# Performance work log

Measured on AMD Instinct MI355X. Metric: run time of the kernel, lower is better.

Reference implementation:

```python
import jax, jax.numpy as jnp
import numpy as np

K = 8
DIM = 64
NUM_BLOCKS = 12
BN_EPS = 1e-5
LRELU_SLOPE = 0.01  # torch nn.LeakyReLU default negative_slope


def knn_indices(xyz, k):
    # xyz: [b, 3, n] -> idx [b, n, k] of k nearest neighbors (self included)
    x = jnp.transpose(xyz, (0, 2, 1))  # [b, n, 3]
    sq = jnp.sum(x * x, axis=-1)  # [b, n]
    d2 = sq[:, :, None] - 2.0 * jnp.einsum('bnd,bmd->bnm', x, x) + sq[:, None, :]
    _, idx = jax.lax.top_k(-d2, k)  # k smallest distances
    return idx


def group_point(points, idx):
    # points [b, d, n], idx [b, n, k] -> grouped [b, d, k, n]
    g = jax.vmap(lambda p, i: p[:, i])(points, idx)  # [b, d, n, k]
    return jnp.transpose(g, (0, 1, 3, 2))


def setup_inputs() -> dict:
    key = jax.random.key(0)
    ks = jax.random.split(key, 6)
    b, n = 8, 4096
    xyz = jax.random.normal(ks[0], (b, 3, n), dtype=jnp.float32)
    points = jax.random.normal(ks[1], (b, DIM, n), dtype=jnp.float32)
    # per-block params (note: the module's second Conv2d per block is never used
    # in forward — layers[4*idx+2] is applied to both center and grouped points)
    conv_w = jax.random.normal(ks[2], (NUM_BLOCKS, DIM, DIM), dtype=jnp.float32) * (1.0 / np.sqrt(DIM))
    conv_b = jax.random.normal(ks[3], (NUM_BLOCKS, DIM), dtype=jnp.float32) * 0.01
    bn_gamma = 1.0 + 0.1 * jax.random.normal(ks[4], (NUM_BLOCKS, DIM), dtype=jnp.float32)
    bn_beta = 0.1 * jax.random.normal(ks[5], (NUM_BLOCKS, DIM), dtype=jnp.float32)
    return {"xyz": xyz, "points": points, "conv_w": conv_w, "conv_b": conv_b,
            "bn_gamma": bn_gamma, "bn_beta": bn_beta}


def reference(xyz, points, conv_w, conv_b, bn_gamma, bn_beta):
    idx = knn_indices(xyz, K)  # fixed graph, computed once in block 0

    def block(p, params):
        w, b, g, be = params  # [DIM,DIM], [DIM], [DIM], [DIM]
        shortcut = p
        # BatchNorm1d (training-mode batch stats over batch & point dims)
        mean = jnp.mean(p, axis=(0, 2), keepdims=True)
        var = jnp.var(p, axis=(0, 2), keepdims=True)
        h = (p - mean) * jax.lax.rsqrt(var + BN_EPS) * g[None, :, None] + be[None, :, None]
        # LeakyReLU
        h = jnp.where(h >= 0, h, LRELU_SLOPE * h)
        # gather neighbor features: [b, d, k, n]
        grouped = group_point(h, idx)
        # shared 1x1 conv on center and grouped points
        center = jnp.einsum('od,bdn->bon', w, h) + b[None, :, None]            # [b,d,n]
        gconv = jnp.einsum('od,bdkn->bokn', w, grouped) + b[None, :, None, None]  # [b,d,k,n]
        # mean over concat([center[:, :, None], gconv], axis=2) == (center + sum_k gconv) / (k+1)
        new_p = (center + jnp.sum(gconv, axis=2)) / (K + 1) + shortcut
        return new_p, None

    out, _ = jax.lax.scan(block, points, (conv_w, conv_b, bn_gamma, bn_beta))
    return out
```

## Files before the change

kernel.cpp:

```cpp
#include <hip/hip_runtime.h>
#include <hip/hip_bf16.h>

#define NB     8
#define NPTS   4096
#define DIMC   64
#define KNN_K  8
#define NBLK   12
#define NREP   8

typedef __attribute__((ext_vector_type(8))) short short8;
typedef __attribute__((ext_vector_type(4))) float f32x4;

__device__ __forceinline__ void bsplit(float v, unsigned short& h, unsigned short& l) {
    unsigned b = __float_as_uint(v);
    h = (unsigned short)(b >> 16);
    float hf = __uint_as_float(b & 0xFFFF0000u);
    float lf = v - hf;
    l = (unsigned short)(__float_as_uint(lf) >> 16);
}

__global__ __launch_bounds__(256) void prep_kernel(
        const float* __restrict__ xyz, float4* __restrict__ pts4g,
        float* __restrict__ stats) {
#pragma clang fp contract(off)
    int g = blockIdx.x * 256 + threadIdx.x;
    if (g < 13 * NREP * 128) stats[g] = 0.0f;
    int b = g >> 12, j = g & 4095;
    const float* xb = xyz + (size_t)b * 3 * NPTS;
    float x = xb[j];
    float y = xb[NPTS + j];
    float z = xb[2 * NPTS + j];
    float sq = (x * x + y * y) + z * z;
    pts4g[g] = make_float4(x, y, z, sq);
}

__global__ __launch_bounds__(256) void cast_kernel(
        const float* __restrict__ pts,
        float* __restrict__ P0, float* __restrict__ stats0) {
    __shared__ __align__(16) float tr[64 * 65];
    __shared__ float slotA[4 * 64], slotB[4 * 64];
    int wg = blockIdx.x;
    int b = wg & 7;
    int n0 = (wg >> 3) << 6;
    int rep = (wg >> 3) & (NREP - 1);
    int tid = threadIdx.x;
    int lane6 = tid & 63;
    int grp = tid >> 6;

    #pragma unroll
    for (int k = 0; k < 16; ++k) {
        int d = grp + (k << 2);
        float v = pts[(((size_t)((b << 6) + d)) << 12) + n0 + lane6];
        tr[d * 65 + lane6] = v;
    }
    __syncthreads();
    int c = lane6;
    float s = 0.0f, s2 = 0.0f;
    #pragma unroll
    for (int k = 0; k < 16; ++k) {
        int p = grp + (k << 2);
        float v = tr[c * 65 + p];
        P0[((size_t)((b << 12) + n0 + p)) * 64 + c] = v;
        s += v; s2 += v * v;
    }
    slotA[grp * 64 + c] = s;
    slotB[grp * 64 + c] = s2;
    __syncthreads();
    if (tid < 64) {
        float t = slotA[tid] + slotA[64 + tid] + slotA[128 + tid] + slotA[192 + tid];
        atomicAdd(&stats0[rep * 128 + tid], t);
    } else if (tid < 128) {
        int cc = tid - 64;
        float t = slotB[cc] + slotB[64 + cc] + slotB[128 + cc] + slotB[192 + cc];
        atomicAdd(&stats0[rep * 128 + 64 + cc], t);
    }
}

#define INS(KEY) do { \
    double key = (KEY); \
    double n0 = fmin(k0, key); \
    double n1 = fmin(k1, fmax(k0, key)); \
    double n2 = fmin(k2, fmax(k1, key)); \
    double n3 = fmin(k3, fmax(k2, key)); \
    double n4 = fmin(k4, fmax(k3, key)); \
    double n5 = fmin(k5, fmax(k4, key)); \
    double n6 = fmin(k6, fmax(k5, key)); \
    double n7 = fmin(k7, fmax(k6, key)); \
    k0 = n0; k1 = n1; k2 = n2; k3 = n3; \
    k4 = n4; k5 = n5; k6 = n6; k7 = n7; } while (0)

__global__ __launch_bounds__(512) void knn_kernel(
        const float4* __restrict__ pts4g, int* __restrict__ idx) {
#pragma clang fp contract(off)
    __shared__ double stash[4 * 9 * 128];
    int wg = blockIdx.x;
    int b = wg >> 5;
    int q0 = (wg & 31) << 7;
    int tid = threadIdx.x;

    int lane  = tid & 63;
    int wave  = tid >> 6;
    int chunk = wave & 3;
    int qgrp  = wave >> 2;
    int q_l   = (qgrp << 6) | lane;

    const float4* cb = pts4g + ((size_t)b << 12);
    float4 qp = cb[q0 + q_l];

    double k0, k1, k2, k3, k4, k5, k6, k7;
    k0 = k1 = k2 = k3 = k4 = k5 = k6 = k7 = __builtin_inf();
    float bd7f = 3.4e38f;

    int chu = __builtin_amdgcn_readfirstlane(chunk);
    const float4* cc = cb + ((size_t)chu << 10);
    int jg0 = chu << 10;

    for (int jo = 0; jo < 128; jo += 8) {
        float d2v[8];
        #pragma unroll
        for (int u = 0; u < 8; ++u) {
            float4 p = cc[jo + u];
            float dot = (qp.x * p.x + qp.y * p.y) + qp.z * p.z;
            d2v[u] = (qp.w - 2.0f * dot) + p.w;
        }
        #pragma unroll
        for (int u = 0; u < 8; ++u) {
            unsigned long long kb =
                __double_as_longlong((double)d2v[u]) |
                (unsigned long long)(jg0 + jo + u);
            INS(__longlong_as_double(kb));
        }
    }
    bd7f = (float)k7;

    for (int jo = 128; jo < 1024; jo += 8) {
        float d2v[8];
        unsigned hm = 0u;
        #pragma unroll
        for (int u = 0; u < 8; ++u) {
            float4 p = cc[jo + u];
            float dot = (qp.x * p.x + qp.y * p.y) + qp.z * p.z;
            float d2 = (qp.w - 2.0f * dot) + p.w;
            d2v[u] = d2;
            hm |= (d2 < bd7f) ? (1u << u) : 0u;
        }
        while (__any(hm != 0u)) {
            if (hm) {
                int u = __builtin_ctz(hm);
                hm &= hm - 1u;
                float t0 = (u & 1) ? d2v[1] : d2v[0];
                float t1 = (u & 1) ? d2v[3] : d2v[2];
                float t2 = (u & 1) ? d2v[5] : d2v[4];
                float t3 = (u & 1) ? d2v[7] : d2v[6];
                float s0 = (u & 2) ? t1 : t0;
                float s1 = (u & 2) ? t3 : t2;
                float d2 = (u & 4) ? s1 : s0;
                unsigned long long kb =
                    __double_as_longlong((double)d2) |
                    (unsigned long long)(jg0 + jo + u);
                INS(__longlong_as_double(kb));
            }
        }
        bd7f = (float)k7;
    }

    {
        double* S = &stash[(chunk * 9) * 128 + q_l];
        S[0 * 128] = k0; S[1 * 128] = k1; S[2 * 128] = k2; S[3 * 128] = k3;
        S[4 * 128] = k4; S[5 * 128] = k5; S[6 * 128] = k6; S[7 * 128] = k7;
        S[8 * 128] = __builtin_inf();
    }
    __syncthreads();

    if (tid < 128) {
        int h0 = 0, h1 = 0, h2 = 0, h3 = 0;
        int* op = idx + ((size_t)(b * NPTS + q0 + tid)) * 8;
        #pragma unroll
        for (int t = 0; t < 8; ++t) {
            double b0 = stash[(0 * 9 + h0) * 128 + tid];
            double b1 = stash[(1 * 9 + h1) * 128 + tid];
            double b2 = stash[(2 * 9 + h2) * 128 + tid];
            double b3 = stash[(3 * 9 + h3) * 128 + tid];
            double best = b0; int bc = 0;
            if (b1 < best) { best = b1; bc = 1; }
            if (b2 < best) { best = b2; bc = 2; }
            if (b3 < best) { best = b3; bc = 3; }
            h0 += (bc == 0); h1 += (bc == 1);
            h2 += (bc == 2); h3 += (bc == 3);
            op[t] = (int)(__double_as_longlong(best) & 0xFFFULL);
        }
    }
}

#define AH_OFF 0
#define AL_OFF (64 * 72)
#define WH_OFF (2 * 64 * 72)
#define WL_OFF (3 * 64 * 72)

__global__ __launch_bounds__(256) void block_kernel(
        const float* __restrict__ Pin, float* __restrict__ Pout,
        const float* __restrict__ statsIn, float* __restrict__ statsOut,
        const float* __restrict__ Wp, const float* __restrict__ Bp,
        const float* __restrict__ Gp, const float* __restrict__ Betap,
        const int* __restrict__ gidx, float* __restrict__ dout, int last) {
    __shared__ __align__(16) unsigned short planes[4 * 64 * 72];
    __shared__ __align__(16) float selft[64 * 64];
    __shared__ __align__(16) int   idxl[64 * 8];
    __shared__ __align__(16) float scale_l[64], shift_l[64], bias_l[64];
    __shared__ float slot[4 * 128];

    int wg = blockIdx.x;
    int b = wg & 7;
    int n0 = (wg >> 3) << 6;
    int rep = (wg >> 3) & (NREP - 1);
    int tid = threadIdx.x;

    const float* Pb = Pin + (((size_t)b) << 18);

    if (tid < 128) {
        ((int4*)idxl)[tid] = ((const int4*)(gidx + ((size_t)(b * NPTS + n0)) * 8))[tid];
    }
    #pragma unroll
    for (int k = 0; k < 4; ++k) {
        int lin = tid + (k << 8);
        ((float4*)selft)[lin] = ((const float4*)&Pb[(size_t)n0 << 6])[lin];
    }
    #pragma unroll
    for (int k = 0; k < 4; ++k) {
        int lin = tid + (k << 8);
        float4 wv = ((const float4*)Wp)[lin];
        int o = lin >> 4, d4 = (lin & 15) << 2;
        unsigned short hx, hy, hz, hw, lx, ly, lz, lw;
        bsplit(wv.x, hx, lx); bsplit(wv.y, hy, ly);
        bsplit(wv.z, hz, lz); bsplit(wv.w, hw, lw);
        *(ushort4*)&planes[WH_OFF + o * 72 + d4] = make_ushort4(hx, hy, hz, hw);
        *(ushort4*)&planes[WL_OFF + o * 72 + d4] = make_ushort4(lx, ly, lz, lw);
    }
    if (tid < 64) {
        int c = tid;
        float sum = 0.0f, sumsq = 0.0f;
        #pragma unroll
        for (int r = 0; r < NREP; ++r) {
            sum   += statsIn[r * 128 + c];
            sumsq += statsIn[r * 128 + 64 + c];
        }
        float mean = sum * (1.0f / 32768.0f);
        float var  = sumsq * (1.0f / 32768.0f) - mean * mean;
        float rs   = 1.0f / sqrtf(var + 1e-5f);
        float sc   = Gp[c] * rs;
        scale_l[c] = sc;
        shift_l[c] = Betap[c] - mean * sc;
        bias_l[c]  = Bp[c];
    }
    __syncthreads();

    {
        int cq = tid & 15;
        int pg = tid >> 4;
        int c4 = cq << 2;
        float4 sc4 = *(const float4*)&scale_l[c4];
        float4 sh4 = *(const float4*)&shift_l[c4];
        #pragma unroll
        for (int i = 0; i < 4; ++i) {
            int pt = (pg << 2) + i;
            int4 ja = *(const int4*)&idxl[pt * 8];
            int4 jb = *(const int4*)&idxl[pt * 8 + 4];
            float4 v[9];
            v[0] = *(const float4*)&selft[(pt << 6) + c4];
            v[1] = *(const float4*)&Pb[(((size_t)ja.x) << 6) + c4];
            v[2] = *(const float4*)&Pb[(((size_t)ja.y) << 6) + c4];
            v[3] = *(const float4*)&Pb[(((size_t)ja.z) << 6) + c4];
            v[4] = *(const float4*)&Pb[(((size_t)ja.w) << 6) + c4];
            v[5] = *(const float4*)&Pb[(((size_t)jb.x) << 6) + c4];
            v[6] = *(const float4*)&Pb[(((size_t)jb.y) << 6) + c4];
            v[7] = *(const float4*)&Pb[(((size_t)jb.z) << 6) + c4];
            v[8] = *(const float4*)&Pb[(((size_t)jb.w) << 6) + c4];
            float4 a = make_float4(0.f, 0.f, 0.f, 0.f);
            #pragma unroll
            for (int k = 0; k < 9; ++k) {
                float hx = v[k].x * sc4.x + sh4.x;
                float hy = v[k].y * sc4.y + sh4.y;
                float hz = v[k].z * sc4.z + sh4.z;
                float hw = v[k].w * sc4.w + sh4.w;
                a.x += fmaxf(hx, 0.01f * hx);
                a.y += fmaxf(hy, 0.01f * hy);
                a.z += fmaxf(hz, 0.01f * hz);
                a.w += fmaxf(hw, 0.01f * hw);
            }
            float mx = a.x * (1.0f / 9.0f), my = a.y * (1.0f / 9.0f);
            float mz = a.z * (1.0f / 9.0f), mw = a.w * (1.0f / 9.0f);
            unsigned short hx2, hy2, hz2, hw2, lx2, ly2, lz2, lw2;
            bsplit(mx, hx2, lx2); bsplit(my, hy2, ly2);
            bsplit(mz, hz2, lz2); bsplit(mw, hw2, lw2);
            *(ushort4*)&planes[AH_OFF + pt * 72 + c4] = make_ushort4(hx2, hy2, hz2, hw2);
            *(ushort4*)&planes[AL_OFF + pt * 72 + c4] = make_ushort4(lx2, ly2, lz2, lw2);
        }
    }
    __syncthreads();

    int lane = tid & 63;
    int w    = tid >> 6;
    int g    = lane >> 4;
    int c    = lane & 15;
    int ptb  = w << 4;

    short8 a_h[2], a_l[2];
    #pragma unroll
    for (int s = 0; s < 2; ++s) {
        int off = (ptb + c) * 72 + (s << 5) + (g << 3);
        a_h[s] = *(const short8*)&planes[AH_OFF + off];
        a_l[s] = *(const short8*)&planes[AL_OFF + off];
    }

    f32x4 out[4];
    #pragma unroll
    for (int ot = 0; ot < 4; ++ot) {
        int co = (ot << 4) + c;
        short8 b_h[2], b_l[2];
        #pragma unroll
        for (int s = 0; s < 2; ++s) {
            int off = co * 72 + (s << 5) + (g << 3);
            b_h[s] = *(const short8*)&planes[WH_OFF + off];
            b_l[s] = *(const short8*)&planes[WL_OFF + off];
        }
        f32x4 acc = {0.f, 0.f, 0.f, 0.f};
        acc = __builtin_amdgcn_mfma_f32_16x16x32_bf16(a_h[0], b_h[0], acc, 0, 0, 0);
        acc = __builtin_amdgcn_mfma_f32_16x16x32_bf16(a_h[1], b_h[1], acc, 0, 0, 0);
        acc = __builtin_amdgcn_mfma_f32_16x16x32_bf16(a_h[0], b_l[0], acc, 0, 0, 0);
        acc = __builtin_amdgcn_mfma_f32_16x16x32_bf16(a_h[1], b_l[1], acc, 0, 0, 0);
        acc = __builtin_amdgcn_mfma_f32_16x16x32_bf16(a_l[0], b_h[0], acc, 0, 0, 0);
        acc = __builtin_amdgcn_mfma_f32_16x16x32_bf16(a_l[1], b_h[1], acc, 0, 0, 0);
        out[ot] = acc;
    }

    #pragma unroll
    for (int ot = 0; ot < 4; ++ot) {
        int co = (ot << 4) + c;
        float bv = bias_l[co];
        #pragma unroll
        for (int j = 0; j < 4; ++j) {
            int pt = ptb + (g << 2) + j;
            out[ot][j] += bv + selft[(pt << 6) + co];
        }
    }

    if (!last) {
        float* PbOut = Pout + ((((size_t)b) << 12) + n0) * 64;
        #pragma unroll
        for (int j = 0; j < 4; ++j) {
            int pt = ptb + (g << 2) + j;
            #pragma unroll
            for (int ot = 0; ot < 4; ++ot)
                PbOut[(size_t)pt * 64 + (ot << 4) + c] = out[ot][j];
        }

        float sv[4], qv[4];
        #pragma unroll
        for (int ot = 0; ot < 4; ++ot) {
            float s = 0.f, q = 0.f;
            #pragma unroll
            for (int j = 0; j < 4; ++j) {
                float v = out[ot][j];
                s += v; q += v * v;
            }
            sv[ot] = s; qv[ot] = q;
        }
        #pragma unroll
        for (int m = 16; m <= 32; m <<= 1) {
            #pragma unroll
            for (int ot = 0; ot < 4; ++ot) {
                sv[ot] += __shfl_xor(sv[ot], m, 64);
                qv[ot] += __shfl_xor(qv[ot], m, 64);
            }
        }
        if (lane < 16) {
            #pragma unroll
            for (int ot = 0; ot < 4; ++ot) {
                slot[w * 128 + (ot << 4) + lane]      = sv[ot];
                slot[w * 128 + 64 + (ot << 4) + lane] = qv[ot];
            }
        }
        __syncthreads();
        if (tid < 128) {
            float t = slot[tid] + slot[128 + tid] + slot[256 + tid] + slot[384 + tid];
            atomicAdd(&statsOut[rep * 128 + tid], t);
        }
    } else {
        __syncthreads();
        float* stage = (float*)planes;
        #pragma unroll
        for (int ot = 0; ot < 4; ++ot) {
            int co = (ot << 4) + c;
            #pragma unroll
            for (int j = 0; j < 4; ++j)
                stage[co * 65 + ptb + (g << 2) + j] = out[ot][j];
        }
        __syncthreads();
        #pragma unroll
        for (int k = 0; k < 16; ++k) {
            int lin = tid + (k << 8);
            int o = lin >> 6, pt = lin & 63;
            dout[(((size_t)((b << 6) + o)) << 12) + n0 + pt] = stage[o * 65 + pt];
        }
    }
}

extern "C" void kernel_launch(void* const* d_in, const int* in_sizes, int n_in,
                              void* d_out, int out_size, void* d_ws, size_t ws_size,
                              hipStream_t stream) {
    const float* xyz    = (const float*)d_in[0];
    const float* pts    = (const float*)d_in[1];
    const float* conv_w = (const float*)d_in[2];
    const float* conv_b = (const float*)d_in[3];
    const float* gamma  = (const float*)d_in[4];
    const float* beta   = (const float*)d_in[5];
    float* out = (float*)d_out;

    char* ws = (char*)d_ws;
    float*  P0    = (float*)(ws);
    float*  P1    = (float*)(ws + (size_t)8 * 1024 * 1024);
    int*    idx   = (int*)  (ws + (size_t)16 * 1024 * 1024);
    float*  stats = (float*)(ws + (size_t)17 * 1024 * 1024);
    float4* pts4g = (float4*)(ws + (size_t)18 * 1024 * 1024);

    prep_kernel<<<128, 256, 0, stream>>>(xyz, pts4g, stats);
    cast_kernel<<<512, 256, 0, stream>>>(pts, P0, stats);
    knn_kernel<<<256, 512, 0, stream>>>(pts4g, idx);

    float* Pbuf[2] = {P0, P1};
    for (int t = 0; t < NBLK; ++t) {
        block_kernel<<<512, 256, 0, stream>>>(
            Pbuf[t & 1], Pbuf[(t + 1) & 1],
            stats + (size_t)t * NREP * 128, stats + (size_t)(t + 1) * NREP * 128,
            conv_w + (size_t)t * 4096, conv_b + (size_t)t * 64,
            gamma + (size_t)t * 64, beta + (size_t)t * 64,
            idx, out, (t == NBLK - 1) ? 1 : 0);
    }
}
```

Measured before the change: 284.9 us.

## Precompute activated bf16 split features and run conv per neighbor before summing

Adds a separate h_kernel that applies BatchNorm and LeakyReLU once per point and writes the bf16 hi/lo planes to global memory. The block kernel then gathers those planes per neighbor and accumulates nine MFMA GEMMs, with the weights pre-split and pre-scaled by 1/9 in prep_kernel. Previously each point's 8 neighbors were normalized and activated redundantly before a single GEMM on the aggregated features. The trade is nine times the MFMA work, 12 extra kernel launches, and an extra global write and read of the h planes per block.

```diff
diff --git a/kernel.cpp b/kernel.cpp
--- a/kernel.cpp
+++ b/kernel.cpp
@@ -21,17 +21,28 @@
 
 __global__ __launch_bounds__(256) void prep_kernel(
         const float* __restrict__ xyz, float4* __restrict__ pts4g,
-        float* __restrict__ stats) {
+        float* __restrict__ stats, const float* __restrict__ conv_w,
+        unsigned short* __restrict__ wq) {
 #pragma clang fp contract(off)
     int g = blockIdx.x * 256 + threadIdx.x;
     if (g < 13 * NREP * 128) stats[g] = 0.0f;
-    int b = g >> 12, j = g & 4095;
-    const float* xb = xyz + (size_t)b * 3 * NPTS;
-    float x = xb[j];
-    float y = xb[NPTS + j];
-    float z = xb[2 * NPTS + j];
-    float sq = (x * x + y * y) + z * z;
-    pts4g[g] = make_float4(x, y, z, sq);
+    {
+        int t = g >> 12, rem = g & 4095;
+        float wv = conv_w[g] * (1.0f / 9.0f);
+        unsigned short h, l;
+        bsplit(wv, h, l);
+        wq[(t << 13) + rem]        = h;
+        wq[(t << 13) + 4096 + rem] = l;
+    }
+    if (g < 32768) {
+        int b = g >> 12, j = g & 4095;
+        const float* xb = xyz + (size_t)b * 3 * NPTS;
+        float x = xb[j];
+        float y = xb[NPTS + j];
+        float z = xb[2 * NPTS + j];
+        float sq = (x * x + y * y) + z * z;
+        pts4g[g] = make_float4(x, y, z, sq);
+    }
 }
 
 __global__ __launch_bounds__(256) void cast_kernel(
@@ -192,50 +203,16 @@
     }
 }
 
-#define AH_OFF 0
-#define AL_OFF (64 * 72)
-#define WH_OFF (2 * 64 * 72)
-#define WL_OFF (3 * 64 * 72)
-
-__global__ __launch_bounds__(256) void block_kernel(
-        const float* __restrict__ Pin, float* __restrict__ Pout,
-        const float* __restrict__ statsIn, float* __restrict__ statsOut,
-        const float* __restrict__ Wp, const float* __restrict__ Bp,
+__global__ __launch_bounds__(256) void h_kernel(
+        const float* __restrict__ P, const float* __restrict__ statsIn,
         const float* __restrict__ Gp, const float* __restrict__ Betap,
-        const int* __restrict__ gidx, float* __restrict__ dout, int last) {
-    __shared__ __align__(16) unsigned short planes[4 * 64 * 72];
-    __shared__ __align__(16) float selft[64 * 64];
-    __shared__ __align__(16) int   idxl[64 * 8];
-    __shared__ __align__(16) float scale_l[64], shift_l[64], bias_l[64];
-    __shared__ float slot[4 * 128];
-
+        unsigned short* __restrict__ hH, unsigned short* __restrict__ hL) {
+    __shared__ float scale_l[64], shift_l[64];
     int wg = blockIdx.x;
     int b = wg & 7;
     int n0 = (wg >> 3) << 6;
-    int rep = (wg >> 3) & (NREP - 1);
     int tid = threadIdx.x;
 
-    const float* Pb = Pin + (((size_t)b) << 18);
-
-    if (tid < 128) {
-        ((int4*)idxl)[tid] = ((const int4*)(gidx + ((size_t)(b * NPTS + n0)) * 8))[tid];
-    }
-    #pragma unroll
-    for (int k = 0; k < 4; ++k) {
-        int lin = tid + (k << 8);
-        ((float4*)selft)[lin] = ((const float4*)&Pb[(size_t)n0 << 6])[lin];
-    }
-    #pragma unroll
-    for (int k = 0; k < 4; ++k) {
-        int lin = tid + (k << 8);
-        float4 wv = ((const float4*)Wp)[lin];
-        int o = lin >> 4, d4 = (lin & 15) << 2;
-        unsigned short hx, hy, hz, hw, lx, ly, lz, lw;
-        bsplit(wv.x, hx, lx); bsplit(wv.y, hy, ly);
-        bsplit(wv.z, hz, lz); bsplit(wv.w, hw, lw);
-        *(ushort4*)&planes[WH_OFF + o * 72 + d4] = make_ushort4(hx, hy, hz, hw);
-        *(ushort4*)&planes[WL_OFF + o * 72 + d4] = make_ushort4(lx, ly, lz, lw);
-    }
     if (tid < 64) {
         int c = tid;
         float sum = 0.0f, sumsq = 0.0f;
@@ -250,51 +227,50 @@
         float sc   = Gp[c] * rs;
         scale_l[c] = sc;
         shift_l[c] = Betap[c] - mean * sc;
-        bias_l[c]  = Bp[c];
     }
     __syncthreads();
 
-    {
-        int cq = tid & 15;
-        int pg = tid >> 4;
-        int c4 = cq << 2;
-        float4 sc4 = *(const float4*)&scale_l[c4];
-        float4 sh4 = *(const float4*)&shift_l[c4];
-        #pragma unroll
-        for (int i = 0; i < 4; ++i) {
-            int pt = (pg << 2) + i;
-            int4 ja = *(const int4*)&idxl[pt * 8];
-            int4 jb = *(const int4*)&idxl[pt * 8 + 4];
-            float4 v[9];
-            v[0] = *(const float4*)&selft[(pt << 6) + c4];
-            v[1] = *(const float4*)&Pb[(((size_t)ja.x) << 6) + c4];
-            v[2] = *(const float4*)&Pb[(((size_t)ja.y) << 6) + c4];
-            v[3] = *(const float4*)&Pb[(((size_t)ja.z) << 6) + c4];
-            v[4] = *(const float4*)&Pb[(((size_t)ja.w) << 6) + c4];
-            v[5] = *(const float4*)&Pb[(((size_t)jb.x) << 6) + c4];
-            v[6] = *(const float4*)&Pb[(((size_t)jb.y) << 6) + c4];
-            v[7] = *(const float4*)&Pb[(((size_t)jb.z) << 6) + c4];
-            v[8] = *(const float4*)&Pb[(((size_t)jb.w) << 6) + c4];
-            float4 a = make_float4(0.f, 0.f, 0.f, 0.f);
-            #pragma unroll
-            for (int k = 0; k < 9; ++k) {
-                float hx = v[k].x * sc4.x + sh4.x;
-                float hy = v[k].y * sc4.y + sh4.y;
-                float hz = v[k].z * sc4.z + sh4.z;
-                float hw = v[k].w * sc4.w + sh4.w;
-                a.x += fmaxf(hx, 0.01f * hx);
-                a.y += fmaxf(hy, 0.01f * hy);
-                a.z += fmaxf(hz, 0.01f * hz);
-                a.w += fmaxf(hw, 0.01f * hw);
-            }
-            float mx = a.x * (1.0f / 9.0f), my = a.y * (1.0f / 9.0f);
-            float mz = a.z * (1.0f / 9.0f), mw = a.w * (1.0f / 9.0f);
-            unsigned short hx2, hy2, hz2, hw2, lx2, ly2, lz2, lw2;
-            bsplit(mx, hx2, lx2); bsplit(my, hy2, ly2);
-            bsplit(mz, hz2, lz2); bsplit(mw, hw2, lw2);
-            *(ushort4*)&planes[AH_OFF + pt * 72 + c4] = make_ushort4(hx2, hy2, hz2, hw2);
-            *(ushort4*)&planes[AL_OFF + pt * 72 + c4] = make_ushort4(lx2, ly2, lz2, lw2);
-        }
+    const float4* P4 = (const float4*)(P + (((size_t)(b << 12) + n0) << 6));
+    ushort4* h4 = (ushort4*)(hH + (((size_t)(b << 12) + n0) << 6));
+    ushort4* l4 = (ushort4*)(hL + (((size_t)(b << 12) + n0) << 6));
+    #pragma unroll
+    for (int k = 0; k < 4; ++k) {
+        int lin = tid + (k << 8);
+        int c4 = (lin & 15) << 2;
+        float4 v = P4[lin];
+        float hx = v.x * scale_l[c4 + 0] + shift_l[c4 + 0];
+        float hy = v.y * scale_l[c4 + 1] + shift_l[c4 + 1];
+        float hz = v.z * scale_l[c4 + 2] + shift_l[c4 + 2];
+        float hw = v.w * scale_l[c4 + 3] + shift_l[c4 + 3];
+        hx = fmaxf(hx, 0.01f * hx); hy = fmaxf(hy, 0.01f * hy);
+        hz = fmaxf(hz, 0.01f * hz); hw = fmaxf(hw, 0.01f * hw);
+        unsigned short ax, ay, az, aw, bx, by, bz, bw;
+        bsplit(hx, ax, bx); bsplit(hy, ay, by);
+        bsplit(hz, az, bz); bsplit(hw, aw, bw);
+        h4[lin] = make_ushort4(ax, ay, az, aw);
+        l4[lin] = make_ushort4(bx, by, bz, bw);
+    }
+}
+
+__global__ __launch_bounds__(256) void block_kernel(
+        const float* __restrict__ Pin, float* __restrict__ Pout,
+        float* __restrict__ statsOut,
+        const unsigned short* __restrict__ whl, const float* __restrict__ Bp,
+        const int* __restrict__ gidx,
+        const unsigned short* __restrict__ hH, const unsigned short* __restrict__ hL,
+        float* __restrict__ dout, int last) {
+    __shared__ __align__(16) int   idxl[64 * 8];
+    __shared__ float slot[4 * 128];
+    __shared__ __align__(16) float stage[64 * 65];
+
+    int wg = blockIdx.x;
+    int b = wg & 7;
+    int n0 = (wg >> 3) << 6;
+    int rep = (wg >> 3) & (NREP - 1);
+    int tid = threadIdx.x;
+
+    if (tid < 128) {
+        ((int4*)idxl)[tid] = ((const int4*)(gidx + ((size_t)(b * NPTS + n0)) * 8))[tid];
     }
     __syncthreads();
 
@@ -302,56 +278,67 @@
     int w    = tid >> 6;
     int g    = lane >> 4;
     int c    = lane & 15;
-    int ptb  = w << 4;
-
-    short8 a_h[2], a_l[2];
-    #pragma unroll
-    for (int s = 0; s < 2; ++s) {
-        int off = (ptb + c) * 72 + (s << 5) + (g << 3);
-        a_h[s] = *(const short8*)&planes[AH_OFF + off];
-        a_l[s] = *(const short8*)&planes[AL_OFF + off];
-    }
-
-    f32x4 out[4];
+    int ptl  = (w << 4) + c;
+
+    int r[9];
+    r[0] = n0 + ptl;
+    #pragma unroll
+    for (int j = 1; j < 9; ++j) r[j] = idxl[ptl * 8 + (j - 1)];
+
+    const unsigned short* hHb = hH + ((size_t)(b << 12) << 6);
+    const unsigned short* hLb = hL + ((size_t)(b << 12) << 6);
+    const unsigned short* whi = whl;
+    const unsigned short* wlo = whl + 4096;
+
+    short8 bh[4][2], bl[4][2];
     #pragma unroll
     for (int ot = 0; ot < 4; ++ot) {
         int co = (ot << 4) + c;
-        short8 b_h[2], b_l[2];
-        #pragma unroll
-        for (int s = 0; s < 2; ++s) {
-            int off = co * 72 + (s << 5) + (g << 3);
-            b_h[s] = *(const short8*)&planes[WH_OFF + off];
-            b_l[s] = *(const short8*)&planes[WL_OFF + off];
-        }
-        f32x4 acc = {0.f, 0.f, 0.f, 0.f};
-        acc = __builtin_amdgcn_mfma_f32_16x16x32_bf16(a_h[0], b_h[0], acc, 0, 0, 0);
-        acc = __builtin_amdgcn_mfma_f32_16x16x32_bf16(a_h[1], b_h[1], acc, 0, 0, 0);
-        acc = __builtin_amdgcn_mfma_f32_16x16x32_bf16(a_h[0], b_l[0], acc, 0, 0, 0);
-        acc = __builtin_amdgcn_mfma_f32_16x16x32_bf16(a_h[1], b_l[1], acc, 0, 0, 0);
-        acc = __builtin_amdgcn_mfma_f32_16x16x32_bf16(a_l[0], b_h[0], acc, 0, 0, 0);
-        acc = __builtin_amdgcn_mfma_f32_16x16x32_bf16(a_l[1], b_h[1], acc, 0, 0, 0);
-        out[ot] = acc;
-    }
-
+        #pragma unroll
+        for (int p = 0; p < 2; ++p) {
+            bh[ot][p] = *(const short8*)&whi[(co << 6) + (p << 5) + (g << 3)];
+            bl[ot][p] = *(const short8*)&wlo[(co << 6) + (p << 5) + (g << 3)];
+        }
+    }
+
+    f32x4 acc[4];
+    #pragma unroll
+    for (int ot = 0; ot < 4; ++ot) acc[ot] = (f32x4){0.f, 0.f, 0.f, 0.f};
+
+    #pragma unroll
+    for (int s = 0; s < 18; ++s) {
+        int j = s >> 1, p = s & 1;
+        int off = (r[j] << 6) + (p << 5) + (g << 3);
+        short8 ah = *(const short8*)&hHb[off];
+        short8 al = *(const short8*)&hLb[off];
+        #pragma unroll
+        for (int ot = 0; ot < 4; ++ot) {
+            acc[ot] = __builtin_amdgcn_mfma_f32_16x16x32_bf16(ah, bh[ot][p], acc[ot], 0, 0, 0);
+            acc[ot] = __builtin_amdgcn_mfma_f32_16x16x32_bf16(ah, bl[ot][p], acc[ot], 0, 0, 0);
+            acc[ot] = __builtin_amdgcn_mfma_f32_16x16x32_bf16(al, bh[ot][p], acc[ot], 0, 0, 0);
+        }
+    }
+
+    const float* Pb = Pin + (((size_t)b) << 18);
     #pragma unroll
     for (int ot = 0; ot < 4; ++ot) {
         int co = (ot << 4) + c;
-        float bv = bias_l[co];
-        #pragma unroll
-        for (int j = 0; j < 4; ++j) {
-            int pt = ptb + (g << 2) + j;
-            out[ot][j] += bv + selft[(pt << 6) + co];
+        float bv = Bp[co];
+        #pragma unroll
+        for (int jj = 0; jj < 4; ++jj) {
+            int ptd = (w << 4) + (g << 2) + jj;
+            acc[ot][jj] += bv + Pb[(((size_t)(n0 + ptd)) << 6) + co];
         }
     }
 
     if (!last) {
         float* PbOut = Pout + ((((size_t)b) << 12) + n0) * 64;
         #pragma unroll
-        for (int j = 0; j < 4; ++j) {
-            int pt = ptb + (g << 2) + j;
+        for (int jj = 0; jj < 4; ++jj) {
+            int ptd = (w << 4) + (g << 2) + jj;
             #pragma unroll
             for (int ot = 0; ot < 4; ++ot)
-                PbOut[(size_t)pt * 64 + (ot << 4) + c] = out[ot][j];
+                PbOut[(size_t)ptd * 64 + (ot << 4) + c] = acc[ot][jj];
         }
 
         float sv[4], qv[4];
@@ -359,8 +346,8 @@
         for (int ot = 0; ot < 4; ++ot) {
             float s = 0.f, q = 0.f;
             #pragma unroll
-            for (int j = 0; j < 4; ++j) {
-                float v = out[ot][j];
+            for (int jj = 0; jj < 4; ++jj) {
+                float v = acc[ot][jj];
                 s += v; q += v * v;
             }
             sv[ot] = s; qv[ot] = q;
@@ -386,14 +373,12 @@
             atomicAdd(&statsOut[rep * 128 + tid], t);
         }
     } else {
-        __syncthreads();
-        float* stage = (float*)planes;
         #pragma unroll
         for (int ot = 0; ot < 4; ++ot) {
             int co = (ot << 4) + c;
             #pragma unroll
-            for (int j = 0; j < 4; ++j)
-                stage[co * 65 + ptb + (g << 2) + j] = out[ot][j];
+            for (int jj = 0; jj < 4; ++jj)
+                stage[co * 65 + (w << 4) + (g << 2) + jj] = acc[ot][jj];
         }
         __syncthreads();
         #pragma unroll
@@ -417,23 +402,28 @@
     float* out = (float*)d_out;
 
     char* ws = (char*)d_ws;
-    float*  P0    = (float*)(ws);
-    float*  P1    = (float*)(ws + (size_t)8 * 1024 * 1024);
-    int*    idx   = (int*)  (ws + (size_t)16 * 1024 * 1024);
-    float*  stats = (float*)(ws + (size_t)17 * 1024 * 1024);
-    float4* pts4g = (float4*)(ws + (size_t)18 * 1024 * 1024);
-
-    prep_kernel<<<128, 256, 0, stream>>>(xyz, pts4g, stats);
+    float*          P0    = (float*)(ws);
+    float*          P1    = (float*)(ws + (size_t)8 * 1024 * 1024);
+    int*            idx   = (int*)  (ws + (size_t)16 * 1024 * 1024);
+    float*          stats = (float*)(ws + (size_t)17 * 1024 * 1024);
+    float4*         pts4g = (float4*)(ws + (size_t)18 * 1024 * 1024);
+    unsigned short* wq    = (unsigned short*)(ws + (size_t)18 * 1024 * 1024 + 512 * 1024);
+    unsigned short* hH    = (unsigned short*)(ws + (size_t)19 * 1024 * 1024);
+    unsigned short* hL    = (unsigned short*)(ws + (size_t)23 * 1024 * 1024);
+
+    prep_kernel<<<192, 256, 0, stream>>>(xyz, pts4g, stats, conv_w, wq);
     cast_kernel<<<512, 256, 0, stream>>>(pts, P0, stats);
     knn_kernel<<<256, 512, 0, stream>>>(pts4g, idx);
 
     float* Pbuf[2] = {P0, P1};
     for (int t = 0; t < NBLK; ++t) {
+        h_kernel<<<512, 256, 0, stream>>>(
+            Pbuf[t & 1], stats + (size_t)t * NREP * 128,
+            gamma + (size_t)t * 64, beta + (size_t)t * 64, hH, hL);
         block_kernel<<<512, 256, 0, stream>>>(
             Pbuf[t & 1], Pbuf[(t + 1) & 1],
-            stats + (size_t)t * NREP * 128, stats + (size_t)(t + 1) * NREP * 128,
-            conv_w + (size_t)t * 4096, conv_b + (size_t)t * 64,
-            gamma + (size_t)t * 64, beta + (size_t)t * 64,
-            idx, out, (t == NBLK - 1) ? 1 : 0);
-    }
-}
+            stats + (size_t)(t + 1) * NREP * 128,
+            wq + (size_t)t * 8192, conv_b + (size_t)t * 64,
+            idx, hH, hL, out, (t == NBLK - 1) ? 1 : 0);
+    }
+}
```

New measurement: 422.7 us. 48.4% more time.

## Sort points by x and prune kNN search with sweep-line early exit

Applied to the files above, without the earlier changes.

Adds a per-batch bitonic sort of points by x-coordinate and rewrites the kNN kernel to scan outward from each query's sorted position. Each side's scan stops once the squared x-gap exceeds the current 8th-best distance, so most of the 4096 candidates are never examined. The original indices are recovered through a permutation array. The cost is an extra serial sort kernel that runs on only 8 workgroups, plus data-dependent loop lengths and divergence. The 1e-3 tolerance on the stopping test is meant to guard against rounding in the distance formula.

```diff
diff --git a/kernel.cpp b/kernel.cpp
--- a/kernel.cpp
+++ b/kernel.cpp
@@ -34,6 +34,178 @@
     pts4g[g] = make_float4(x, y, z, sq);
 }
 
+__global__ __launch_bounds__(512) void sort_kernel(
+        const float4* __restrict__ pts4g, float4* __restrict__ spts,
+        int* __restrict__ perm) {
+    __shared__ unsigned long long keys[4096];
+    int b = blockIdx.x;
+    int tid = threadIdx.x;
+    const float4* src = pts4g + ((size_t)b << 12);
+
+    #pragma unroll
+    for (int t = 0; t < 8; ++t) {
+        int i = tid + (t << 9);
+        unsigned s = __float_as_uint(src[i].x);
+        unsigned m = (s & 0x80000000u) ? ~s : (s | 0x80000000u);
+        keys[i] = ((unsigned long long)m << 12) | (unsigned)i;
+    }
+    __syncthreads();
+
+    for (int k = 2; k <= 4096; k <<= 1) {
+        for (int j = k >> 1; j > 0; j >>= 1) {
+            #pragma unroll 2
+            for (int t = 0; t < 4; ++t) {
+                int p = tid + (t << 9);
+                int i = ((p & ~(j - 1)) << 1) | (p & (j - 1));
+                int ixj = i | j;
+                bool up = ((i & k) == 0);
+                unsigned long long a = keys[i], c = keys[ixj];
+                if ((a > c) == up) { keys[i] = c; keys[ixj] = a; }
+            }
+            __syncthreads();
+        }
+    }
+
+    #pragma unroll
+    for (int t = 0; t < 8; ++t) {
+        int i = tid + (t << 9);
+        int oi = (int)(keys[i] & 0xFFFULL);
+        spts[((size_t)b << 12) + i] = src[oi];
+        perm[((size_t)b << 12) + i] = oi;
+    }
+}
+
+#define INS(KEY) do { \
+    double key = (KEY); \
+    double n0 = fmin(k0, key); \
+    double n1 = fmin(k1, fmax(k0, key)); \
+    double n2 = fmin(k2, fmax(k1, key)); \
+    double n3 = fmin(k3, fmax(k2, key)); \
+    double n4 = fmin(k4, fmax(k3, key)); \
+    double n5 = fmin(k5, fmax(k4, key)); \
+    double n6 = fmin(k6, fmax(k5, key)); \
+    double n7 = fmin(k7, fmax(k6, key)); \
+    k0 = n0; k1 = n1; k2 = n2; k3 = n3; \
+    k4 = n4; k5 = n5; k6 = n6; k7 = n7; } while (0)
+
+#define PROC(POS, SIDE) do { \
+    const float4* cg = sb + (POS); \
+    const int* pgq = pb + (POS); \
+    int pi0 = pgq[0], pi1 = pgq[1], pi2 = pgq[2], pi3 = pgq[3]; \
+    int pi4 = pgq[4], pi5 = pgq[5], pi6 = pgq[6], pi7 = pgq[7]; \
+    float d2v[8]; unsigned hm = 0u; float gxf = 0.f, gxl = 0.f; \
+    _Pragma("unroll") \
+    for (int u = 0; u < 8; ++u) { \
+        float4 p = cg[u]; \
+        if (u == 0) gxf = p.x; \
+        if (u == 7) gxl = p.x; \
+        float dot = (qp.x * p.x + qp.y * p.y) + qp.z * p.z; \
+        float d2 = (qp.w - 2.0f * dot) + p.w; \
+        d2v[u] = d2; \
+        hm |= (d2 < bd7f) ? (1u << u) : 0u; \
+    } \
+    while (__any(hm != 0u)) { \
+        if (hm) { \
+            int u = __builtin_ctz(hm); hm &= hm - 1u; \
+            float t0 = (u & 1) ? d2v[1] : d2v[0]; \
+            float t1 = (u & 1) ? d2v[3] : d2v[2]; \
+            float t2 = (u & 1) ? d2v[5] : d2v[4]; \
+            float t3 = (u & 1) ? d2v[7] : d2v[6]; \
+            float s0 = (u & 2) ? t1 : t0; \
+            float s1 = (u & 2) ? t3 : t2; \
+            float d2s = (u & 4) ? s1 : s0; \
+            int i0 = (u & 1) ? pi1 : pi0; \
+            int i1 = (u & 1) ? pi3 : pi2; \
+            int i2 = (u & 1) ? pi5 : pi4; \
+            int i3 = (u & 1) ? pi7 : pi6; \
+            int j0 = (u & 2) ? i1 : i0; \
+            int j1 = (u & 2) ? i3 : i2; \
+            int ci = (u & 4) ? j1 : j0; \
+            unsigned long long kb = \
+                __double_as_longlong((double)d2s) | (unsigned long long)ci; \
+            INS(__longlong_as_double(kb)); \
+        } \
+    } \
+    bd7f = (float)k7; \
+    if ((SIDE) == 1) { float dx = gxl - qp.x; doneR = doneR | (dx * dx > bd7f + 1e-3f); } \
+    if ((SIDE) == 2) { float dx = qp.x - gxf; doneL = doneL | (dx * dx > bd7f + 1e-3f); } \
+} while (0)
+
+__global__ __launch_bounds__(512) void knn_kernel(
+        const float4* __restrict__ spts, const int* __restrict__ perm,
+        int* __restrict__ idx) {
+#pragma clang fp contract(off)
+    __shared__ double stash[8 * 9 * 64];
+    int wg = blockIdx.x;
+    int b = wg >> 5;
+    int qbase = (wg & 31) << 7;
+    int tid = threadIdx.x;
+    int lane = tid & 63;
+    int wave = tid >> 6;
+    int grp = wave >> 2;
+    int chunk = wave & 3;
+
+    const float4* sb = spts + ((size_t)b << 12);
+    const int* pb = perm + ((size_t)b << 12);
+
+    int qs0 = qbase + (grp << 6);
+    float4 qp = sb[qs0 + lane];
+
+    double k0, k1, k2, k3, k4, k5, k6, k7;
+    k0 = k1 = k2 = k3 = k4 = k5 = k6 = k7 = __builtin_inf();
+    float bd7f = 3.4e38f;
+
+    int chu = __builtin_amdgcn_readfirstlane(chunk);
+    int qsu = __builtin_amdgcn_readfirstlane(qs0);
+
+    int doneR = 0, doneL = 0;
+
+    PROC(qsu + (chu << 3), 0);
+    PROC(qsu + ((chu + 4) << 3), 0);
+
+    int rpos = qsu + 64 + (chu << 3);
+    int lpos = qsu - ((chu + 1) << 3);
+    for (;;) {
+        bool actR = (rpos < 4096) && __any(doneR == 0);
+        bool actL = (lpos >= 0) && __any(doneL == 0);
+        if (!actR && !actL) break;
+        if (actR) { PROC(rpos, 1); rpos += 32; }
+        if (actL) { PROC(lpos, 2); lpos -= 32; }
+    }
+
+    {
+        double* S = &stash[(wave * 9) * 64 + lane];
+        S[0 * 64] = k0; S[1 * 64] = k1; S[2 * 64] = k2; S[3 * 64] = k3;
+        S[4 * 64] = k4; S[5 * 64] = k5; S[6 * 64] = k6; S[7 * 64] = k7;
+        S[8 * 64] = __builtin_inf();
+    }
+    __syncthreads();
+
+    if (tid < 128) {
+        int g = tid >> 6, l = tid & 63;
+        int sq = qbase + (g << 6) + l;
+        int oq = pb[sq];
+        int* op = idx + ((size_t)(b * NPTS + oq)) * 8;
+        int s0b = (g * 4 + 0) * 9, s1b = (g * 4 + 1) * 9;
+        int s2b = (g * 4 + 2) * 9, s3b = (g * 4 + 3) * 9;
+        int h0 = 0, h1 = 0, h2 = 0, h3 = 0;
+        #pragma unroll
+        for (int t = 0; t < 8; ++t) {
+            double c0 = stash[(s0b + h0) * 64 + l];
+            double c1 = stash[(s1b + h1) * 64 + l];
+            double c2 = stash[(s2b + h2) * 64 + l];
+            double c3 = stash[(s3b + h3) * 64 + l];
+            double best = c0; int bc = 0;
+            if (c1 < best) { best = c1; bc = 1; }
+            if (c2 < best) { best = c2; bc = 2; }
+            if (c3 < best) { best = c3; bc = 3; }
+            h0 += (bc == 0); h1 += (bc == 1);
+            h2 += (bc == 2); h3 += (bc == 3);
+            op[t] = (int)(__double_as_longlong(best) & 0xFFFULL);
+        }
+    }
+}
+
 __global__ __launch_bounds__(256) void cast_kernel(
         const float* __restrict__ pts,
         float* __restrict__ P0, float* __restrict__ stats0) {
@@ -73,122 +245,6 @@
         int cc = tid - 64;
         float t = slotB[cc] + slotB[64 + cc] + slotB[128 + cc] + slotB[192 + cc];
         atomicAdd(&stats0[rep * 128 + 64 + cc], t);
-    }
-}
-
-#define INS(KEY) do { \
-    double key = (KEY); \
-    double n0 = fmin(k0, key); \
-    double n1 = fmin(k1, fmax(k0, key)); \
-    double n2 = fmin(k2, fmax(k1, key)); \
-    double n3 = fmin(k3, fmax(k2, key)); \
-    double n4 = fmin(k4, fmax(k3, key)); \
-    double n5 = fmin(k5, fmax(k4, key)); \
-    double n6 = fmin(k6, fmax(k5, key)); \
-    double n7 = fmin(k7, fmax(k6, key)); \
-    k0 = n0; k1 = n1; k2 = n2; k3 = n3; \
-    k4 = n4; k5 = n5; k6 = n6; k7 = n7; } while (0)
-
-__global__ __launch_bounds__(512) void knn_kernel(
-        const float4* __restrict__ pts4g, int* __restrict__ idx) {
-#pragma clang fp contract(off)
-    __shared__ double stash[4 * 9 * 128];
-    int wg = blockIdx.x;
-    int b = wg >> 5;
-    int q0 = (wg & 31) << 7;
-    int tid = threadIdx.x;
-
-    int lane  = tid & 63;
-    int wave  = tid >> 6;
-    int chunk = wave & 3;
-    int qgrp  = wave >> 2;
-    int q_l   = (qgrp << 6) | lane;
-
-    const float4* cb = pts4g + ((size_t)b << 12);
-    float4 qp = cb[q0 + q_l];
-
-    double k0, k1, k2, k3, k4, k5, k6, k7;
-    k0 = k1 = k2 = k3 = k4 = k5 = k6 = k7 = __builtin_inf();
-    float bd7f = 3.4e38f;
-
-    int chu = __builtin_amdgcn_readfirstlane(chunk);
-    const float4* cc = cb + ((size_t)chu << 10);
-    int jg0 = chu << 10;
-
-    for (int jo = 0; jo < 128; jo += 8) {
-        float d2v[8];
-        #pragma unroll
-        for (int u = 0; u < 8; ++u) {
-            float4 p = cc[jo + u];
-            float dot = (qp.x * p.x + qp.y * p.y) + qp.z * p.z;
-            d2v[u] = (qp.w - 2.0f * dot) + p.w;
-        }
-        #pragma unroll
-        for (int u = 0; u < 8; ++u) {
-            unsigned long long kb =
-                __double_as_longlong((double)d2v[u]) |
-                (unsigned long long)(jg0 + jo + u);
-            INS(__longlong_as_double(kb));
-        }
-    }
-    bd7f = (float)k7;
-
-    for (int jo = 128; jo < 1024; jo += 8) {
-        float d2v[8];
-        unsigned hm = 0u;
-        #pragma unroll
-        for (int u = 0; u < 8; ++u) {
-            float4 p = cc[jo + u];
-            float dot = (qp.x * p.x + qp.y * p.y) + qp.z * p.z;
-            float d2 = (qp.w - 2.0f * dot) + p.w;
-            d2v[u] = d2;
-            hm |= (d2 < bd7f) ? (1u << u) : 0u;
-        }
-        while (__any(hm != 0u)) {
-            if (hm) {
-                int u = __builtin_ctz(hm);
-                hm &= hm - 1u;
-                float t0 = (u & 1) ? d2v[1] : d2v[0];
-                float t1 = (u & 1) ? d2v[3] : d2v[2];
-                float t2 = (u & 1) ? d2v[5] : d2v[4];
-                float t3 = (u & 1) ? d2v[7] : d2v[6];
-                float s0 = (u & 2) ? t1 : t0;
-                float s1 = (u & 2) ? t3 : t2;
-                float d2 = (u & 4) ? s1 : s0;
-                unsigned long long kb =
-                    __double_as_longlong((double)d2) |
-                    (unsigned long long)(jg0 + jo + u);
-                INS(__longlong_as_double(kb));
-            }
-        }
-        bd7f = (float)k7;
-    }
-
-    {
-        double* S = &stash[(chunk * 9) * 128 + q_l];
-        S[0 * 128] = k0; S[1 * 128] = k1; S[2 * 128] = k2; S[3 * 128] = k3;
-        S[4 * 128] = k4; S[5 * 128] = k5; S[6 * 128] = k6; S[7 * 128] = k7;
-        S[8 * 128] = __builtin_inf();
-    }
-    __syncthreads();
-
-    if (tid < 128) {
-        int h0 = 0, h1 = 0, h2 = 0, h3 = 0;
-        int* op = idx + ((size_t)(b * NPTS + q0 + tid)) * 8;
-        #pragma unroll
-        for (int t = 0; t < 8; ++t) {
-            double b0 = stash[(0 * 9 + h0) * 128 + tid];
-            double b1 = stash[(1 * 9 + h1) * 128 + tid];
-            double b2 = stash[(2 * 9 + h2) * 128 + tid];
-            double b3 = stash[(3 * 9 + h3) * 128 + tid];
-            double best = b0; int bc = 0;
-            if (b1 < best) { best = b1; bc = 1; }
-            if (b2 < best) { best = b2; bc = 2; }
-            if (b3 < best) { best = b3; bc = 3; }
-            h0 += (bc == 0); h1 += (bc == 1);
-            h2 += (bc == 2); h3 += (bc == 3);
-            op[t] = (int)(__double_as_longlong(best) & 0xFFFULL);
-        }
     }
 }
 
@@ -422,10 +478,13 @@
     int*    idx   = (int*)  (ws + (size_t)16 * 1024 * 1024);
     float*  stats = (float*)(ws + (size_t)17 * 1024 * 1024);
     float4* pts4g = (float4*)(ws + (size_t)18 * 1024 * 1024);
+    float4* spts  = (float4*)(ws + (size_t)19 * 1024 * 1024);
+    int*    perm  = (int*)  (ws + (size_t)19 * 1024 * 1024 + 512 * 1024);
 
     prep_kernel<<<128, 256, 0, stream>>>(xyz, pts4g, stats);
+    sort_kernel<<<8, 512, 0, stream>>>(pts4g, spts, perm);
     cast_kernel<<<512, 256, 0, stream>>>(pts, P0, stats);
-    knn_kernel<<<256, 512, 0, stream>>>(pts4g, idx);
+    knn_kernel<<<256, 512, 0, stream>>>(spts, perm, idx);
 
     float* Pbuf[2] = {P0, P1};
     for (int t = 0; t < NBLK; ++t) {
```

Result: slower. 318.5 us (+11.8%).
